# Performance work log

Measured on AMD Instinct MI355X. Metric: run time of the kernel, lower is better.

## Reference

```python
import math
import jax, jax.numpy as jnp
import numpy as np

NEG_BIG = -1e12  # matches torch's -1000000000000.0 padding


def setup_inputs() -> dict:
    key = jax.random.key(0)
    k1, k2, k3 = jax.random.split(key, 3)
    bs, n_tok, n_heads, width = 1, 4096, 8, 64
    dst_mxlen, src_mxlen = 32, 64
    q = jax.random.normal(k1, (bs, n_tok, n_heads, width), dtype=jnp.float32)
    k = jax.random.normal(k2, (bs, n_tok, n_heads, width), dtype=jnp.float32)
    v = jax.random.normal(k3, (bs, n_tok, n_heads, width), dtype=jnp.float32)
    # Sliding-window COO: each dst attends to its dst_mxlen preceding tokens (clipped).
    dst = jnp.repeat(jnp.arange(n_tok, dtype=jnp.int32), dst_mxlen)
    cnt = jnp.tile(jnp.arange(dst_mxlen, dtype=jnp.int32), n_tok)
    src = jnp.clip(dst - cnt, 0, n_tok - 1)
    coo = jnp.stack([dst, src, cnt], axis=1)  # [cl, 3]
    return {"v": v, "q": q, "k": k, "coo": coo,
            "dst_mxlen": dst_mxlen, "src_mxlen": src_mxlen, "use_softmax": 1}


def reference(v, q, k, coo, dst_mxlen, src_mxlen, use_softmax):
    bs, n_tok, n_heads, width = q.shape
    cl = coo.shape[0]
    # [b, h, t, w] layout
    qq = jnp.transpose(q, (0, 2, 1, 3))[:, :, coo[:, 0], :]  # [b,h,cl,w]
    kk = jnp.transpose(k, (0, 2, 1, 3))[:, :, coo[:, 1], :]
    vv = jnp.transpose(v, (0, 2, 1, 3))
    scale = -1.0 / math.sqrt(width)
    ww = jnp.sum(jnp.abs(qq - kk), axis=-1) * scale  # [b,h,cl]
    # Padded softmax buffer, last slot is the (optional) softmax denominator pad.
    attn = jnp.full((bs, n_heads, n_tok, dst_mxlen + 1), NEG_BIG, dtype=q.dtype)
    attn = attn.at[:, :, coo[:, 0], coo[:, 2]].set(ww)
    if use_softmax:
        attn = attn.at[:, :, :, -1].set(0.0)
        attn_sm = jax.nn.softmax(attn, axis=-1)
    else:
        attn_sm = jnp.exp(attn)
    attn_sm = attn_sm[:, :, :, :-1]  # [b,h,t,s]
    # Scatter V into the padded buffer: vw[b,h,dst,cnt,:] = vv[b,h,src,:]
    vw = jnp.zeros((bs, n_heads, n_tok, dst_mxlen, width), dtype=q.dtype)
    vw = vw.at[:, :, coo[:, 0], coo[:, 2], :].set(vv[:, :, coo[:, 1], :])
    vo = jnp.einsum('bhds,bhdsw->bdhw', attn_sm, vw)
    return vo
```

## Files before the change

### kernel.cpp

```cpp
#include <hip/hip_runtime.h>
#include <math.h>


typedef float v2f __attribute__((ext_vector_type(2)));

constexpr int H   = 8;
constexpr int W   = 64;
constexpr int TPW = 2;
constexpr int SB  = 4;

template <int CTRL>
__device__ __forceinline__ float dpp_add(float x) {
    int xi = __builtin_bit_cast(int, x);
    int yi = __builtin_amdgcn_update_dpp(0, xi, CTRL, 0xf, 0xf, true);
    return x + __builtin_bit_cast(float, yi);
}

__device__ __forceinline__ float reduce16(float a) {
    a = dpp_add<0xB1>(a);
    a = dpp_add<0x4E>(a);
    a = dpp_add<0x141>(a);
    a = dpp_add<0x140>(a);
    return a;
}

__device__ __forceinline__ float absdiff4(float4 qv, float4 kv) {
    v2f q01 = {qv.x, qv.y}, q23 = {qv.z, qv.w};
    v2f k01 = {kv.x, kv.y}, k23 = {kv.z, kv.w};
    v2f d0 = q01 - k01, d1 = q23 - k23;
    v2f a0 = __builtin_elementwise_max(d0, -d0);
    v2f a1 = __builtin_elementwise_max(d1, -d1);
    v2f ss = a0 + a1;
    return ss.x + ss.y;
}

__global__ __launch_bounds__(256) void l1attn_sparse_kernel(
    const float* __restrict__ v,
    const float* __restrict__ q,
    const float* __restrict__ k,
    const int*   __restrict__ p_dst_mxlen,
    const int*   __restrict__ p_use_softmax,
    float*       __restrict__ out,
    int n_tok)
{
    const int dst_mxlen = *p_dst_mxlen;
    const int use_sm    = *p_use_softmax;

    int bid = blockIdx.x;
    if ((gridDim.x & 7) == 0) {
        const int chunk = gridDim.x >> 3;
        bid = (bid & 7) * chunk + (bid >> 3);
    }

    const int wid  = bid * (blockDim.x >> 6) + (threadIdx.x >> 6);
    const int lane = threadIdx.x & 63;

    const int pairIdx = wid >> 1;
    const int t0 = pairIdx * TPW;
    if (t0 >= n_tok) return;
    const int hh = wid & 1;

    const int h     = hh * 4 + (lane >> 4);
    const int dbase = (lane & 15) * 4;
    const int hoff  = h * W + dbase;

    float4 qv[TPW];
    #pragma unroll
    for (int j = 0; j < TPW; ++j) {
        int t = t0 + j; t = t < n_tok ? t : n_tok - 1;
        qv[j] = *reinterpret_cast<const float4*>(q + t * (H * W) + hoff);
    }

    v2f   acc01[TPW], acc23[TPW];
    float sump[TPW];
    #pragma unroll
    for (int j = 0; j < TPW; ++j) {
        acc01[j] = (v2f){0.f, 0.f}; acc23[j] = (v2f){0.f, 0.f}; sump[j] = 0.f;
    }

    if (t0 - (dst_mxlen - 1) <= 0) {
        const float4 kv = *reinterpret_cast<const float4*>(k + hoff);
        const float4 vv = *reinterpret_cast<const float4*>(v + hoff);
        v2f v01 = {vv.x, vv.y}, v23 = {vv.z, vv.w};
        #pragma unroll
        for (int j = 0; j < TPW; ++j) {
            const int t = t0 + j;
            float a = reduce16(absdiff4(qv[j], kv));
            int mm = dst_mxlen - t; mm = mm > 0 ? mm : 0;
            const float p = (float)mm * __expf(a * -0.125f);
            sump[j] += p;
            acc01[j] += p * v01;
            acc23[j] += p * v23;
        }
    }

    int s_lo = t0 - (dst_mxlen - 1); s_lo = s_lo < 1 ? 1 : s_lo;
    int s_hi = t0 + TPW - 1; s_hi = s_hi < n_tok - 1 ? s_hi : n_tok - 1;

    for (int sbase = s_lo; sbase <= s_hi; sbase += SB) {
        float4 kb[SB], vb[SB];
        #pragma unroll
        for (int e = 0; e < SB; ++e) {
            int su = sbase + e;
            int sa = su < n_tok ? su : n_tok - 1;
            const int base = sa * (H * W) + hoff;
            kb[e] = *reinterpret_cast<const float4*>(k + base);
            vb[e] = *reinterpret_cast<const float4*>(v + base);
        }
        #pragma unroll
        for (int e = 0; e < SB; ++e) {
            const int su = sbase + e;
            v2f v01 = {vb[e].x, vb[e].y}, v23 = {vb[e].z, vb[e].w};
            #pragma unroll
            for (int j = 0; j < TPW; ++j) {
                const int t = t0 + j;
                float a = reduce16(absdiff4(qv[j], kb[e]));
                const float m =
                    ((unsigned)(t - su) < (unsigned)dst_mxlen) ? 1.f : 0.f;
                const float p = m * __expf(a * -0.125f);
                sump[j] += p;
                acc01[j] += p * v01;
                acc23[j] += p * v23;
            }
        }
    }

    #pragma unroll
    for (int j = 0; j < TPW; ++j) {
        const int t = t0 + j;
        if (t < n_tok) {
            const float scale = use_sm ? 1.0f / (1.0f + sump[j]) : 1.0f;
            float4 o = {acc01[j].x * scale, acc01[j].y * scale,
                        acc23[j].x * scale, acc23[j].y * scale};
            *reinterpret_cast<float4*>(out + t * (H * W) + hoff) = o;
        }
    }
}

extern "C" void kernel_launch(void* const* d_in, const int* in_sizes, int n_in,
                              void* d_out, int out_size, void* d_ws, size_t ws_size,
                              hipStream_t stream) {
    const float* v   = (const float*)d_in[0];
    const float* q   = (const float*)d_in[1];
    const float* k   = (const float*)d_in[2];
    const int*   p_dst_mxlen = (const int*)d_in[4];
    const int*   p_use_sm    = (const int*)d_in[6];
    float* out = (float*)d_out;

    const int n_tok = in_sizes[1] / (H * W);

    const int pairs  = (n_tok + TPW - 1) / TPW;
    const int waves  = pairs * 2;
    const int blocks = (waves + 3) / 4;
    l1attn_sparse_kernel<<<blocks, 256, 0, stream>>>(
        v, q, k, p_dst_mxlen, p_use_sm, out, n_tok);
}
```

Baseline: 22.01 us.

## Split source window across two waves per token pair and reduce via LDS

Each block now handles one token pair, and two waves per head-half each process half of the 33-source window. The partial accumulators and softmax sums are combined through shared memory after a barrier. A fully unrolled fast path for dst_mxlen==32 drops the per-source mask, and the block count doubles. This shortens the serial per-wave loop and raises parallelism, at the cost of an LDS round-trip, a __syncthreads and more blocks.

```diff
diff --git a/kernel.cpp b/kernel.cpp
--- a/kernel.cpp
+++ b/kernel.cpp
@@ -7,7 +7,6 @@
 constexpr int H   = 8;
 constexpr int W   = 64;
 constexpr int TPW = 2;
-constexpr int SB  = 4;
 
 template <int CTRL>
 __device__ __forceinline__ float dpp_add(float x) {
@@ -34,7 +33,7 @@
     return ss.x + ss.y;
 }
 
-__global__ __launch_bounds__(256) void l1attn_sparse_kernel(
+__global__ __launch_bounds__(256, 8) void l1attn_sparse_kernel(
     const float* __restrict__ v,
     const float* __restrict__ q,
     const float* __restrict__ k,
@@ -52,13 +51,13 @@
         bid = (bid & 7) * chunk + (bid >> 3);
     }
 
-    const int wid  = bid * (blockDim.x >> 6) + (threadIdx.x >> 6);
+    const int sub  = threadIdx.x >> 6;
     const int lane = threadIdx.x & 63;
+    const int hh   = sub >> 1;
+    const int wh   = sub & 1;
 
-    const int pairIdx = wid >> 1;
-    const int t0 = pairIdx * TPW;
+    const int t0 = bid * TPW;
     if (t0 >= n_tok) return;
-    const int hh = wid & 1;
 
     const int h     = hh * 4 + (lane >> 4);
     const int dbase = (lane & 15) * 4;
@@ -78,45 +77,68 @@
         acc01[j] = (v2f){0.f, 0.f}; acc23[j] = (v2f){0.f, 0.f}; sump[j] = 0.f;
     }
 
-    if (t0 - (dst_mxlen - 1) <= 0) {
-        const float4 kv = *reinterpret_cast<const float4*>(k + hoff);
-        const float4 vv = *reinterpret_cast<const float4*>(v + hoff);
+    auto body_both = [&](int s) {
+        const int base = s * (H * W) + hoff;
+        const float4 kv = *reinterpret_cast<const float4*>(k + base);
+        const float4 vv = *reinterpret_cast<const float4*>(v + base);
         v2f v01 = {vv.x, vv.y}, v23 = {vv.z, vv.w};
         #pragma unroll
         for (int j = 0; j < TPW; ++j) {
-            const int t = t0 + j;
             float a = reduce16(absdiff4(qv[j], kv));
-            int mm = dst_mxlen - t; mm = mm > 0 ? mm : 0;
-            const float p = (float)mm * __expf(a * -0.125f);
+            const float p = __expf(a * -0.125f);
             sump[j] += p;
             acc01[j] += p * v01;
             acc23[j] += p * v23;
         }
-    }
+    };
+    auto body_one = [&](int s, int j) {
+        const int base = s * (H * W) + hoff;
+        const float4 kv = *reinterpret_cast<const float4*>(k + base);
+        const float4 vv = *reinterpret_cast<const float4*>(v + base);
+        v2f v01 = {vv.x, vv.y}, v23 = {vv.z, vv.w};
+        float a = reduce16(absdiff4(qv[j], kv));
+        const float p = __expf(a * -0.125f);
+        sump[j] += p;
+        acc01[j] += p * v01;
+        acc23[j] += p * v23;
+    };
 
-    int s_lo = t0 - (dst_mxlen - 1); s_lo = s_lo < 1 ? 1 : s_lo;
-    int s_hi = t0 + TPW - 1; s_hi = s_hi < n_tok - 1 ? s_hi : n_tok - 1;
+    if (dst_mxlen == 32 && t0 >= 32 && t0 + 1 <= n_tok - 1) {
+        if (wh == 0) {
+            const int sA = t0 - 31;
+            body_one(sA, 1 - 1);
+            #pragma unroll
+            for (int i = 1; i <= 16; ++i) body_both(sA + i);
+        } else {
+            const int sB = t0 - 14;
+            #pragma unroll
+            for (int i = 0; i < 15; ++i) body_both(sB + i);
+            body_one(t0 + 1, 1);
+        }
+    } else {
+        int s_lo = t0 - (dst_mxlen - 1); s_lo = s_lo < 0 ? 0 : s_lo;
+        int s_hi = t0 + TPW - 1; s_hi = s_hi < n_tok - 1 ? s_hi : n_tok - 1;
+        const int len  = s_hi - s_lo + 1;
+        const int half = (len + 1) >> 1;
+        const int my_lo = wh ? s_lo + half : s_lo;
+        const int my_hi = wh ? s_hi       : s_lo + half - 1;
 
-    for (int sbase = s_lo; sbase <= s_hi; sbase += SB) {
-        float4 kb[SB], vb[SB];
-        #pragma unroll
-        for (int e = 0; e < SB; ++e) {
-            int su = sbase + e;
-            int sa = su < n_tok ? su : n_tok - 1;
-            const int base = sa * (H * W) + hoff;
-            kb[e] = *reinterpret_cast<const float4*>(k + base);
-            vb[e] = *reinterpret_cast<const float4*>(v + base);
-        }
-        #pragma unroll
-        for (int e = 0; e < SB; ++e) {
-            const int su = sbase + e;
-            v2f v01 = {vb[e].x, vb[e].y}, v23 = {vb[e].z, vb[e].w};
+        for (int s = my_lo; s <= my_hi; ++s) {
+            const int base = s * (H * W) + hoff;
+            const float4 kv = *reinterpret_cast<const float4*>(k + base);
+            const float4 vv = *reinterpret_cast<const float4*>(v + base);
+            v2f v01 = {vv.x, vv.y}, v23 = {vv.z, vv.w};
             #pragma unroll
             for (int j = 0; j < TPW; ++j) {
                 const int t = t0 + j;
-                float a = reduce16(absdiff4(qv[j], kb[e]));
-                const float m =
-                    ((unsigned)(t - su) < (unsigned)dst_mxlen) ? 1.f : 0.f;
+                float a = reduce16(absdiff4(qv[j], kv));
+                float m;
+                if (s == 0) {
+                    int mm = dst_mxlen - t;
+                    m = (float)(mm > 0 ? mm : 0);
+                } else {
+                    m = ((unsigned)(t - s) < (unsigned)dst_mxlen) ? 1.f : 0.f;
+                }
                 const float p = m * __expf(a * -0.125f);
                 sump[j] += p;
                 acc01[j] += p * v01;
@@ -125,14 +147,34 @@
         }
     }
 
-    #pragma unroll
-    for (int j = 0; j < TPW; ++j) {
-        const int t = t0 + j;
-        if (t < n_tok) {
-            const float scale = use_sm ? 1.0f / (1.0f + sump[j]) : 1.0f;
-            float4 o = {acc01[j].x * scale, acc01[j].y * scale,
-                        acc23[j].x * scale, acc23[j].y * scale};
-            *reinterpret_cast<float4*>(out + t * (H * W) + hoff) = o;
+    __shared__ float lds[2][TPW][5][64];
+    if (wh == 1) {
+        #pragma unroll
+        for (int j = 0; j < TPW; ++j) {
+            lds[hh][j][0][lane] = acc01[j].x;
+            lds[hh][j][1][lane] = acc01[j].y;
+            lds[hh][j][2][lane] = acc23[j].x;
+            lds[hh][j][3][lane] = acc23[j].y;
+            lds[hh][j][4][lane] = sump[j];
+        }
+    }
+    __syncthreads();
+    if (wh == 0) {
+        #pragma unroll
+        for (int j = 0; j < TPW; ++j) {
+            acc01[j].x += lds[hh][j][0][lane];
+            acc01[j].y += lds[hh][j][1][lane];
+            acc23[j].x += lds[hh][j][2][lane];
+            acc23[j].y += lds[hh][j][3][lane];
+            sump[j]    += lds[hh][j][4][lane];
+
+            const int t = t0 + j;
+            if (t < n_tok) {
+                const float scale = use_sm ? 1.0f / (1.0f + sump[j]) : 1.0f;
+                float4 o = {acc01[j].x * scale, acc01[j].y * scale,
+                            acc23[j].x * scale, acc23[j].y * scale};
+                *reinterpret_cast<float4*>(out + t * (H * W) + hoff) = o;
+            }
         }
     }
 }
@@ -149,9 +191,7 @@
 
     const int n_tok = in_sizes[1] / (H * W);
 
-    const int pairs  = (n_tok + TPW - 1) / TPW;
-    const int waves  = pairs * 2;
-    const int blocks = (waves + 3) / 4;
+    const int blocks = (n_tok + TPW - 1) / TPW;
     l1attn_sparse_kernel<<<blocks, 256, 0, stream>>>(
         v, q, k, p_dst_mxlen, p_use_sm, out, n_tok);
 }
```

New measurement: 27.01 us. 22.7% more time.
